# Kernel optimization log

Hardware: AMD Instinct MI355X
Metric: run time of the kernel (lower is better)

The kernel has to match this reference:

```python
import jax, jax.numpy as jnp
import numpy as np

H, DH = 8, 64          # num_heads, head_dim
DM = H * DH            # hidden_dim = 512
LAM = 1.0              # lambda_param
SCALE = 1.0 / np.sqrt(DH)


def setup_inputs() -> dict:
    key = jax.random.key(0)
    ks = jax.random.split(key, 12)
    B, N, R = 2, 2048, 16
    s = DM ** -0.5
    inp = {
        "x": jax.random.normal(ks[0], (B, N, DM), jnp.float32),
        "pde_residuals": jax.random.normal(ks[1], (B, N, R), jnp.float32),
        "mask": jnp.ones((B, 1, N, N), jnp.int32),
        "Wq": jax.random.normal(ks[2], (DM, DM), jnp.float32) * s,
        "bq": jax.random.normal(ks[3], (DM,), jnp.float32) * 0.01,
        "Wk": jax.random.normal(ks[4], (DM, DM), jnp.float32) * s,
        "bk": jax.random.normal(ks[5], (DM,), jnp.float32) * 0.01,
        "Wv": jax.random.normal(ks[6], (DM, DM), jnp.float32) * s,
        "bv": jax.random.normal(ks[7], (DM,), jnp.float32) * 0.01,
        "Wo": jax.random.normal(ks[8], (DM, DM), jnp.float32) * s,
        "bo": jax.random.normal(ks[9], (DM,), jnp.float32) * 0.01,
    }
    return inp


def reference(x, pde_residuals, mask, Wq, bq, Wk, bk, Wv, bv, Wo, bo):
    B, N, _ = x.shape
    # torch nn.Linear: y = x @ W.T + b
    q = (x @ Wq.T + bq).reshape(B, N, H, DH)
    k = (x @ Wk.T + bk).reshape(B, N, H, DH)
    v = (x @ Wv.T + bv).reshape(B, N, H, DH)
    # [B,H,N,N]
    scores = jnp.einsum('bqhd,bkhd->bhqk', q, k) * SCALE
    # residual bias: rb.unsqueeze(1) - rb.unsqueeze(2) -> bias[b,i,j] = rb[b,j] - rb[b,i]
    rb = jnp.linalg.norm(pde_residuals, axis=-1)            # [B,N]
    bias = rb[:, None, None, :] - rb[:, None, :, None]       # [B,1,N,N]
    scores = scores - LAM * bias
    scores = jnp.where(mask == 0, -jnp.inf, scores)
    attn = jax.nn.softmax(scores, axis=-1)                   # dropout is identity in eval
    out = jnp.einsum('bhqk,bkhd->bqhd', attn, v).reshape(B, N, DM)
    return out @ Wo.T + bo
```

## Files before the change

### kernel.cpp

```cpp
#include <hip/hip_runtime.h>
#include <hip/hip_bf16.h>
#include <math.h>

#define B_ 2
#define N_ 2048
#define H_ 8
#define DH_ 64
#define DM_ 512
#define R_ 16
#define LAM_ 1.0f
#define SCALE_ 0.125f

typedef unsigned short u16;
typedef unsigned int u32;
typedef u16 u16x4 __attribute__((ext_vector_type(4)));
typedef u16 u16x8 __attribute__((ext_vector_type(8)));
typedef __bf16 bf16x8 __attribute__((ext_vector_type(8)));
typedef float f32x4 __attribute__((ext_vector_type(4)));

static __device__ __forceinline__ u16 f2bf(float f) {
    union { float f; unsigned u; } v; v.f = f;
    unsigned r = v.u + 0x7FFF + ((v.u >> 16) & 1);
    return (u16)(r >> 16);
}

static __device__ __forceinline__ u32 pack_bf16(float lo, float hi) {
    float2 f2; f2.x = lo; f2.y = hi;
    __hip_bfloat162 h2 = __float22bfloat162_rn(f2);
    u32 r;
    __builtin_memcpy(&r, &h2, 4);
    return r;
}

static __device__ __forceinline__ void gl_lds16(const void* g, void* l) {
    __builtin_amdgcn_global_load_lds(
        (const __attribute__((address_space(1))) unsigned*)g,
        (__attribute__((address_space(3))) unsigned*)l, 16, 0, 0);
}

__global__ __launch_bounds__(256) void cast_all(
    const float* __restrict__ x, const float* __restrict__ wq,
    const float* __restrict__ wk, const float* __restrict__ wv,
    const float* __restrict__ wo, u16* __restrict__ xb, u16* __restrict__ wqb,
    u16* __restrict__ wkb, u16* __restrict__ wvb, u16* __restrict__ wob) {
    int y = blockIdx.y;
    const float* src; u16* dst; int n;
    switch (y) {
        case 0: src = x;  dst = xb;  n = 2097152; break;
        case 1: src = wq; dst = wqb; n = 262144;  break;
        case 2: src = wk; dst = wkb; n = 262144;  break;
        case 3: src = wv; dst = wvb; n = 262144;  break;
        default: src = wo; dst = wob; n = 262144; break;
    }
    int i = (blockIdx.x * 256 + threadIdx.x) * 8;
    if (i >= n) return;
    float4 a = *(const float4*)(src + i);
    float4 b = *(const float4*)(src + i + 4);
    u16x8 o;
    o[0] = f2bf(a.x); o[1] = f2bf(a.y); o[2] = f2bf(a.z); o[3] = f2bf(a.w);
    o[4] = f2bf(b.x); o[5] = f2bf(b.y); o[6] = f2bf(b.z); o[7] = f2bf(b.w);
    *(u16x8*)(dst + i) = o;
}

__global__ void rb_kernel(const float* __restrict__ pde, float* __restrict__ rbs) {
    int i = blockIdx.x * blockDim.x + threadIdx.x;
    if (i >= B_ * N_) return;
    const float4* p = (const float4*)(pde + (size_t)i * R_);
    float s = 0.f;
#pragma unroll
    for (int j = 0; j < 4; ++j) {
        float4 v = p[j];
        s += v.x * v.x + v.y * v.y + v.z * v.z + v.w * v.w;
    }
    rbs[i] = LAM_ * sqrtf(s);
}

__global__ __launch_bounds__(256) void mask_scan(const int* __restrict__ mask,
                                                 int* __restrict__ flags) {
    int kt = blockIdx.x, qt = blockIdx.y, b = blockIdx.z;
    __shared__ int red;
    if (threadIdx.x == 0) red = 0;
    __syncthreads();
    int any = 0;
    for (int c = threadIdx.x; c < 1024; c += 256) {
        int row = c >> 4, seg = c & 15;
        int4 m4 = *(const int4*)(mask + (size_t)b * N_ * N_ +
                                 (size_t)(qt * 64 + row) * N_ + kt * 64 + seg * 4);
        any |= (m4.x == 0) | (m4.y == 0) | (m4.z == 0) | (m4.w == 0);
    }
    if (__ballot(any)) {
        if ((threadIdx.x & 63) == 0) atomicOr(&red, 1);
    }
    __syncthreads();
    if (threadIdx.x == 0) flags[(b * 32 + qt) * 32 + kt] = red;
}

struct Acc2 { f32x4 v[4][2]; };

static __device__ __forceinline__ Acc2 gemm_core2(const u16* __restrict__ A,
                                                  const u16* __restrict__ W,
                                                  int m0, int nn0, char* LDSB) {
    int t = threadIdx.x, l = t & 63, w = t >> 6;
    int lg = l >> 4, li = l & 15;
    int wr = w >> 1, wc = w & 1;
    Acc2 acc;
#pragma unroll
    for (int m = 0; m < 4; ++m)
#pragma unroll
        for (int n = 0; n < 2; ++n) acc.v[m][n] = (f32x4){0.f, 0.f, 0.f, 0.f};

    int srl = l >> 3;
    int colb = ((l & 7) * 16) ^ (srl << 4);

    for (int k0 = 0; k0 < DM_; k0 += 64) {
        __syncthreads();
#pragma unroll
        for (int i = 0; i < 4; ++i) {
            int c = w * 4 + i;
            int row = c * 8 + srl;
            gl_lds16(A + (size_t)(m0 + row) * DM_ + k0 + (colb >> 1),
                     LDSB + c * 1024);
        }
#pragma unroll
        for (int i = 0; i < 2; ++i) {
            int c = w * 2 + i;
            int row = c * 8 + srl;
            gl_lds16(W + (size_t)(nn0 + row) * DM_ + k0 + (colb >> 1),
                     LDSB + 16384 + c * 1024);
        }
        __syncthreads();
#pragma unroll
        for (int kk = 0; kk < 2; ++kk) {
            bf16x8 af[4], bfr[2];
#pragma unroll
            for (int m = 0; m < 4; ++m) {
                int r = wr * 64 + m * 16 + li;
                af[m] = *(const bf16x8*)(LDSB + r * 128 +
                                         ((kk * 64 + lg * 16) ^ ((r & 7) << 4)));
            }
#pragma unroll
            for (int n = 0; n < 2; ++n) {
                int r = wc * 32 + n * 16 + li;
                bfr[n] = *(const bf16x8*)(LDSB + 16384 + r * 128 +
                                          ((kk * 64 + lg * 16) ^ ((r & 7) << 4)));
            }
#pragma unroll
            for (int m = 0; m < 4; ++m)
#pragma unroll
                for (int n = 0; n < 2; ++n)
                    acc.v[m][n] = __builtin_amdgcn_mfma_f32_16x16x32_bf16(
                        af[m], bfr[n], acc.v[m][n], 0, 0, 0);
        }
    }
    return acc;
}

__global__ __launch_bounds__(256) void gemm_qkv(
    const u16* __restrict__ xb, const u16* __restrict__ wqb,
    const u16* __restrict__ wkb, const u16* __restrict__ wvb,
    const float* __restrict__ bq, const float* __restrict__ bk,
    const float* __restrict__ bv, u16* __restrict__ q_bf,
    u16* __restrict__ k_bf, u16* __restrict__ vt) {
    __shared__ char LDSB[24576];
    int y = blockIdx.y;
    int which = y >> 3;
    int nn0 = (y & 7) * 64;
    const u16* W = which == 0 ? wqb : which == 1 ? wkb : wvb;
    const float* bias = which == 0 ? bq : which == 1 ? bk : bv;
    int m0 = blockIdx.x * 128;
    Acc2 acc = gemm_core2(xb, W, m0, nn0, LDSB);

    int t = threadIdx.x, l = t & 63, w = t >> 6;
    int lg = l >> 4, li = l & 15;
    int wr = w >> 1, wc = w & 1;
    float scale = which == 0 ? SCALE_ : 1.0f;
#pragma unroll
    for (int n = 0; n < 2; ++n) {
        int col = nn0 + wc * 32 + n * 16 + li;
        float bv_ = bias[col];
        if (which < 2) {
            u16* dst = which == 0 ? q_bf : k_bf;
#pragma unroll
            for (int m = 0; m < 4; ++m)
#pragma unroll
                for (int r = 0; r < 4; ++r) {
                    int row = m0 + wr * 64 + m * 16 + lg * 4 + r;
                    dst[(size_t)row * DM_ + col] =
                        f2bf((acc.v[m][n][r] + bv_) * scale);
                }
        } else {
            int h = col >> 6, d = col & 63;
#pragma unroll
            for (int m = 0; m < 4; ++m) {
                int row = m0 + wr * 64 + m * 16 + lg * 4;
                int b = row >> 11, nb = row & (N_ - 1);
                u16x4 o;
#pragma unroll
                for (int r = 0; r < 4; ++r) o[r] = f2bf(acc.v[m][n][r] + bv_);
                *(u16x4*)(vt + ((size_t)((b * 8 + h) * 64 + d)) * N_ + nb) = o;
            }
        }
    }
}

__global__ __launch_bounds__(256) void gemm_out(
    const u16* __restrict__ aob, const u16* __restrict__ wob,
    const float* __restrict__ bo, float* __restrict__ out) {
    __shared__ char LDSB[24576];
    int nn0 = blockIdx.y * 64;
    int m0 = blockIdx.x * 128;
    Acc2 acc = gemm_core2(aob, wob, m0, nn0, LDSB);

    int t = threadIdx.x, l = t & 63, w = t >> 6;
    int lg = l >> 4, li = l & 15;
    int wr = w >> 1, wc = w & 1;
#pragma unroll
    for (int n = 0; n < 2; ++n) {
        int col = nn0 + wc * 32 + n * 16 + li;
        float bv_ = bo[col];
#pragma unroll
        for (int m = 0; m < 4; ++m)
#pragma unroll
            for (int r = 0; r < 4; ++r) {
                int row = m0 + wr * 64 + m * 16 + lg * 4 + r;
                out[(size_t)row * DM_ + col] = acc.v[m][n][r] + bv_;
            }
    }
}

__global__ __launch_bounds__(512) void attn8(
    const u16* __restrict__ qb, const u16* __restrict__ kb,
    const u16* __restrict__ vtb, const float* __restrict__ rbs,
    const int* __restrict__ mask, const int* __restrict__ flags,
    u16* __restrict__ aob) {
    __shared__ char KVB[2][2][16384];
    __shared__ char PsB[8][2048];

    int t = threadIdx.x, l = t & 63, w = t >> 6;
    int g2 = w >> 2, wq = w & 3;
    int raw = blockIdx.x;
    int sid = (raw & 7) * 64 + (raw >> 3);
    int bh = sid >> 5, qg = sid & 31;
    int b = bh >> 3, h = bh & 7;
    int m0 = qg * 64 + wq * 16;
    int lg = l >> 4, li = l & 15;
    int k0base = g2 * 1024;

    int srl = l >> 3;
    int colb = ((l & 7) * 16) ^ (srl << 4);

    bf16x8 qa[2];
    {
        const u16* qrow = qb + (size_t)(b * N_ + m0 + li) * DM_ + h * DH_;
        qa[0] = __builtin_bit_cast(bf16x8, *(const u16x8*)(qrow + lg * 8));
        qa[1] = __builtin_bit_cast(bf16x8, *(const u16x8*)(qrow + 32 + lg * 8));
    }

    f32x4 o[4];
#pragma unroll
    for (int dt = 0; dt < 4; ++dt) o[dt] = (f32x4){0.f, 0.f, 0.f, 0.f};
    float mrun = -INFINITY, lrun = 0.f;

    auto STAGE = [&](int bufi, int k0s) {
        char* base = &KVB[g2][bufi][0];
#pragma unroll
        for (int c = 0; c < 2; ++c) {
            int chunk = wq * 2 + c;
            int row = chunk * 8 + srl;
            gl_lds16(kb + (size_t)(b * N_ + k0s + row) * DM_ + h * DH_ + (colb >> 1),
                     base + chunk * 1024);
            gl_lds16(vtb + ((size_t)(bh * DH_ + row)) * N_ + k0s + (colb >> 1),
                     base + 8192 + chunk * 1024);
        }
    };

    STAGE(0, k0base);
    __syncthreads();

    char* pwbase = &PsB[w][0] + li * 16 + ((lg & 1) << 3);
    int slot_lohi = (lg >> 1);

    int buf = 0;
    for (int tt = 0; tt < 16; ++tt) {
        int k0 = k0base + tt * 64;
        if (tt < 15) STAGE(buf ^ 1, k0 + 64);

        const char* Kb = &KVB[g2][buf][0];
        const char* Vb = &KVB[g2][buf][8192];
        int flag = flags[(b * 32 + qg) * 32 + (k0 >> 6)];

        f32x4 st[4];
        __builtin_amdgcn_s_setprio(1);
#pragma unroll
        for (int kt = 0; kt < 4; ++kt) {
            st[kt] = (f32x4){0.f, 0.f, 0.f, 0.f};
#pragma unroll
            for (int s = 0; s < 2; ++s) {
                int key = kt * 16 + li;
                bf16x8 kf = *(const bf16x8*)(Kb + key * 128 +
                                             ((s * 64 + lg * 16) ^ ((key & 7) << 4)));
                st[kt] = __builtin_amdgcn_mfma_f32_16x16x32_bf16(kf, qa[s], st[kt],
                                                                 0, 0, 0);
            }
        }
        __builtin_amdgcn_s_setprio(0);

#pragma unroll
        for (int kt = 0; kt < 4; ++kt) {
            float4 rb4 = *(const float4*)(rbs + b * N_ + k0 + kt * 16 + lg * 4);
            st[kt][0] -= rb4.x; st[kt][1] -= rb4.y;
            st[kt][2] -= rb4.z; st[kt][3] -= rb4.w;
        }
        if (flag) {
#pragma unroll
            for (int kt = 0; kt < 4; ++kt)
#pragma unroll
                for (int r = 0; r < 4; ++r) {
                    int rowg = m0 + li;
                    int keyg = k0 + kt * 16 + lg * 4 + r;
                    if (mask[(size_t)b * N_ * N_ + (size_t)rowg * N_ + keyg] == 0)
                        st[kt][r] = -INFINITY;
                }
        }

        float m0_ = fmaxf(fmaxf(st[0][0], st[0][1]), fmaxf(st[0][2], st[0][3]));
        float m1_ = fmaxf(fmaxf(st[1][0], st[1][1]), fmaxf(st[1][2], st[1][3]));
        float m2_ = fmaxf(fmaxf(st[2][0], st[2][1]), fmaxf(st[2][2], st[2][3]));
        float m3_ = fmaxf(fmaxf(st[3][0], st[3][1]), fmaxf(st[3][2], st[3][3]));
        float pmax = fmaxf(fmaxf(m0_, m1_), fmaxf(m2_, m3_));
        pmax = fmaxf(pmax, __shfl_xor(pmax, 16));
        pmax = fmaxf(pmax, __shfl_xor(pmax, 32));

        if (!__all(pmax - mrun <= 8.0f)) {
            float mnew = fmaxf(fmaxf(mrun, pmax), -3.0e38f);
            float corr = __expf(mrun - mnew);
            mrun = mnew;
            lrun *= corr;
#pragma unroll
            for (int dt = 0; dt < 4; ++dt)
#pragma unroll
                for (int r = 0; r < 4; ++r) o[dt][r] *= corr;
        }

        float ps[8];
#pragma unroll
        for (int kt = 0; kt < 4; ++kt) {
            float p0 = __expf(st[kt][0] - mrun);
            float p1 = __expf(st[kt][1] - mrun);
            float p2 = __expf(st[kt][2] - mrun);
            float p3 = __expf(st[kt][3] - mrun);
            ps[kt * 2 + 0] = p0 + p1;
            ps[kt * 2 + 1] = p2 + p3;
            uint2 pkw;
            pkw.x = pack_bf16(p0, p1);
            pkw.y = pack_bf16(p2, p3);
            int slot = (kt >> 1) * 4 + (kt & 1) * 2 + slot_lohi;
            *(uint2*)(pwbase + (slot << 8)) = pkw;
        }
        float psum = ((ps[0] + ps[1]) + (ps[2] + ps[3])) +
                     ((ps[4] + ps[5]) + (ps[6] + ps[7]));
        psum += __shfl_xor(psum, 16);
        psum += __shfl_xor(psum, 32);
        lrun += psum;

        bf16x8 pf[2];
#pragma unroll
        for (int s = 0; s < 2; ++s)
            pf[s] = *(const bf16x8*)(&PsB[w][0] + ((s * 4 + lg) << 8) + li * 16);
        __builtin_amdgcn_s_setprio(1);
#pragma unroll
        for (int dt = 0; dt < 4; ++dt)
#pragma unroll
            for (int s = 0; s < 2; ++s) {
                int d = dt * 16 + li;
                bf16x8 vf = *(const bf16x8*)(Vb + d * 128 +
                                             ((s * 64 + lg * 16) ^ ((d & 7) << 4)));
                o[dt] = __builtin_amdgcn_mfma_f32_16x16x32_bf16(vf, pf[s], o[dt],
                                                                0, 0, 0);
            }
        __builtin_amdgcn_s_setprio(0);

        __syncthreads();
        buf ^= 1;
    }

    float* cmb = (float*)&KVB[0][0][0];
    float* mlc = (float*)&PsB[0][0];
    if (g2 == 1) {
        float* dst = cmb + wq * 1024;
#pragma unroll
        for (int dt = 0; dt < 4; ++dt)
            *(f32x4*)(dst + li * 64 + dt * 16 + lg * 4) = o[dt];
        if (lg == 0) {
            float2 ml; ml.x = mrun; ml.y = lrun;
            *(float2*)(mlc + (wq * 16 + li) * 2) = ml;
        }
    }
    __syncthreads();
    if (g2 == 0) {
        float2 ml1 = *(const float2*)(mlc + (wq * 16 + li) * 2);
        float m = fmaxf(mrun, ml1.x);
        float w0 = __expf(mrun - m), w1 = __expf(ml1.x - m);
        float denom = 1.f / (lrun * w0 + ml1.y * w1);
        w0 *= denom; w1 *= denom;
        const float* src = cmb + wq * 1024;
        u16* orow = aob + (size_t)(b * N_ + m0 + li) * DM_ + h * DH_;
#pragma unroll
        for (int dt = 0; dt < 4; ++dt) {
            f32x4 p1 = *(const f32x4*)(src + li * 64 + dt * 16 + lg * 4);
            u16x4 ov;
#pragma unroll
            for (int r = 0; r < 4; ++r)
                ov[r] = f2bf(o[dt][r] * w0 + p1[r] * w1);
            *(u16x4*)(orow + dt * 16 + lg * 4) = ov;
        }
    }
}

extern "C" void kernel_launch(void* const* d_in, const int* in_sizes, int n_in,
                              void* d_out, int out_size, void* d_ws, size_t ws_size,
                              hipStream_t stream) {
    const float* x   = (const float*)d_in[0];
    const float* pde = (const float*)d_in[1];
    const int*   msk = (const int*)d_in[2];
    const float* Wq  = (const float*)d_in[3];
    const float* bq  = (const float*)d_in[4];
    const float* Wk  = (const float*)d_in[5];
    const float* bk  = (const float*)d_in[6];
    const float* Wv  = (const float*)d_in[7];
    const float* bv  = (const float*)d_in[8];
    const float* Wo  = (const float*)d_in[9];
    const float* bo  = (const float*)d_in[10];
    float* out = (float*)d_out;

    const size_t MAT = (size_t)B_ * N_ * DM_;
    const size_t WSZ = (size_t)DM_ * DM_;
    u16* xb   = (u16*)d_ws;
    u16* q_bf = xb + MAT;
    u16* k_bf = q_bf + MAT;
    u16* vt   = k_bf + MAT;
    u16* aob  = vt + MAT;
    u16* wqb  = aob + MAT;
    u16* wkb  = wqb + WSZ;
    u16* wvb  = wkb + WSZ;
    u16* wob  = wvb + WSZ;
    float* rbs = (float*)(wob + WSZ);
    int* flags = (int*)(rbs + B_ * N_);

    cast_all<<<dim3(1024, 5), 256, 0, stream>>>(x, Wq, Wk, Wv, Wo,
                                                xb, wqb, wkb, wvb, wob);
    rb_kernel<<<(B_ * N_ + 255) / 256, 256, 0, stream>>>(pde, rbs);
    mask_scan<<<dim3(32, 32, 2), 256, 0, stream>>>(msk, flags);

    gemm_qkv<<<dim3(32, 24), 256, 0, stream>>>(xb, wqb, wkb, wvb,
                                               bq, bk, bv, q_bf, k_bf, vt);

    attn8<<<512, 512, 0, stream>>>(q_bf, k_bf, vt, rbs, msk, flags, aob);

    gemm_out<<<dim3(32, 8), 256, 0, stream>>>(aob, wob, bo, out);
}
```

Baseline: 76.93 us.

## Fuse prep kernels into one launch, shrink output GEMM tile, pad combine LDS

The cast, residual-norm and mask-scan kernels are merged into a single prep launch dispatched by blockIdx.y, which removes two kernel launches and their gaps. The output projection GEMM now uses a 64x64 tile with a new gemm_core, doubling the grid from 256 to 512 blocks so more CUs are busy. The attention combine buffer gets a row stride of 68 floats instead of 64 to reduce LDS bank conflicts. Smaller GEMM tiles cut per-block data reuse, and the fused prep kernel launches blocks that exit immediately in the mostly empty y rows.

```diff
diff --git a/kernel.cpp b/kernel.cpp
--- a/kernel.cpp
+++ b/kernel.cpp
@@ -38,61 +38,117 @@
         (__attribute__((address_space(3))) unsigned*)l, 16, 0, 0);
 }
 
-__global__ __launch_bounds__(256) void cast_all(
+__global__ __launch_bounds__(256) void prep(
     const float* __restrict__ x, const float* __restrict__ wq,
     const float* __restrict__ wk, const float* __restrict__ wv,
-    const float* __restrict__ wo, u16* __restrict__ xb, u16* __restrict__ wqb,
-    u16* __restrict__ wkb, u16* __restrict__ wvb, u16* __restrict__ wob) {
-    int y = blockIdx.y;
-    const float* src; u16* dst; int n;
-    switch (y) {
-        case 0: src = x;  dst = xb;  n = 2097152; break;
-        case 1: src = wq; dst = wqb; n = 262144;  break;
-        case 2: src = wk; dst = wkb; n = 262144;  break;
-        case 3: src = wv; dst = wvb; n = 262144;  break;
-        default: src = wo; dst = wob; n = 262144; break;
-    }
-    int i = (blockIdx.x * 256 + threadIdx.x) * 8;
-    if (i >= n) return;
-    float4 a = *(const float4*)(src + i);
-    float4 b = *(const float4*)(src + i + 4);
-    u16x8 o;
-    o[0] = f2bf(a.x); o[1] = f2bf(a.y); o[2] = f2bf(a.z); o[3] = f2bf(a.w);
-    o[4] = f2bf(b.x); o[5] = f2bf(b.y); o[6] = f2bf(b.z); o[7] = f2bf(b.w);
-    *(u16x8*)(dst + i) = o;
-}
-
-__global__ void rb_kernel(const float* __restrict__ pde, float* __restrict__ rbs) {
-    int i = blockIdx.x * blockDim.x + threadIdx.x;
-    if (i >= B_ * N_) return;
-    const float4* p = (const float4*)(pde + (size_t)i * R_);
-    float s = 0.f;
-#pragma unroll
-    for (int j = 0; j < 4; ++j) {
-        float4 v = p[j];
-        s += v.x * v.x + v.y * v.y + v.z * v.z + v.w * v.w;
-    }
-    rbs[i] = LAM_ * sqrtf(s);
-}
-
-__global__ __launch_bounds__(256) void mask_scan(const int* __restrict__ mask,
-                                                 int* __restrict__ flags) {
-    int kt = blockIdx.x, qt = blockIdx.y, b = blockIdx.z;
-    __shared__ int red;
-    if (threadIdx.x == 0) red = 0;
-    __syncthreads();
-    int any = 0;
-    for (int c = threadIdx.x; c < 1024; c += 256) {
-        int row = c >> 4, seg = c & 15;
-        int4 m4 = *(const int4*)(mask + (size_t)b * N_ * N_ +
-                                 (size_t)(qt * 64 + row) * N_ + kt * 64 + seg * 4);
-        any |= (m4.x == 0) | (m4.y == 0) | (m4.z == 0) | (m4.w == 0);
-    }
-    if (__ballot(any)) {
-        if ((threadIdx.x & 63) == 0) atomicOr(&red, 1);
-    }
-    __syncthreads();
-    if (threadIdx.x == 0) flags[(b * 32 + qt) * 32 + kt] = red;
+    const float* __restrict__ wo, const float* __restrict__ pde,
+    const int* __restrict__ mask, u16* __restrict__ xb, u16* __restrict__ wqb,
+    u16* __restrict__ wkb, u16* __restrict__ wvb, u16* __restrict__ wob,
+    float* __restrict__ rbs, int* __restrict__ flags) {
+    int y = blockIdx.y, bx = blockIdx.x, t = threadIdx.x;
+
+    if (y <= 4) {
+        const float* src; u16* dst; int n;
+        switch (y) {
+            case 0: src = x;  dst = xb;  n = 2097152; break;
+            case 1: src = wq; dst = wqb; n = 262144;  break;
+            case 2: src = wk; dst = wkb; n = 262144;  break;
+            case 3: src = wv; dst = wvb; n = 262144;  break;
+            default: src = wo; dst = wob; n = 262144; break;
+        }
+        int i = (bx * 256 + t) * 8;
+        if (i >= n) return;
+        float4 a = *(const float4*)(src + i);
+        float4 b = *(const float4*)(src + i + 4);
+        u16x8 o;
+        o[0] = f2bf(a.x); o[1] = f2bf(a.y); o[2] = f2bf(a.z); o[3] = f2bf(a.w);
+        o[4] = f2bf(b.x); o[5] = f2bf(b.y); o[6] = f2bf(b.z); o[7] = f2bf(b.w);
+        *(u16x8*)(dst + i) = o;
+    } else if (y == 5) {
+        int i = bx * 256 + t;
+        if (i >= B_ * N_) return;
+        const float4* p = (const float4*)(pde + (size_t)i * R_);
+        float s = 0.f;
+#pragma unroll
+        for (int j = 0; j < 4; ++j) {
+            float4 v = p[j];
+            s += v.x * v.x + v.y * v.y + v.z * v.z + v.w * v.w;
+        }
+        rbs[i] = LAM_ * sqrtf(s);
+    } else {
+        int b = y - 6;
+        int qt = bx >> 5, kt = bx & 31;
+        __shared__ int red;
+        if (t == 0) red = 0;
+        __syncthreads();
+        int any = 0;
+        for (int c = t; c < 1024; c += 256) {
+            int row = c >> 4, seg = c & 15;
+            int4 m4 = *(const int4*)(mask + (size_t)b * N_ * N_ +
+                                     (size_t)(qt * 64 + row) * N_ + kt * 64 + seg * 4);
+            any |= (m4.x == 0) | (m4.y == 0) | (m4.z == 0) | (m4.w == 0);
+        }
+        if (__ballot(any)) {
+            if ((t & 63) == 0) atomicOr(&red, 1);
+        }
+        __syncthreads();
+        if (t == 0) flags[(b * 32 + qt) * 32 + kt] = red;
+    }
+}
+
+struct Acc { f32x4 v[2][2]; };
+
+static __device__ __forceinline__ Acc gemm_core(const u16* __restrict__ A,
+                                                const u16* __restrict__ W,
+                                                int m0, int nn0, char* LDSB) {
+    int t = threadIdx.x, l = t & 63, w = t >> 6;
+    int lg = l >> 4, li = l & 15;
+    int wr = w >> 1, wc = w & 1;
+    Acc acc;
+#pragma unroll
+    for (int m = 0; m < 2; ++m)
+#pragma unroll
+        for (int n = 0; n < 2; ++n) acc.v[m][n] = (f32x4){0.f, 0.f, 0.f, 0.f};
+
+    int srl = l >> 3;
+    int colb = ((l & 7) * 16) ^ (srl << 4);
+
+    for (int k0 = 0; k0 < DM_; k0 += 64) {
+        __syncthreads();
+#pragma unroll
+        for (int i = 0; i < 2; ++i) {
+            int c = w * 2 + i;
+            int row = c * 8 + srl;
+            gl_lds16(A + (size_t)(m0 + row) * DM_ + k0 + (colb >> 1),
+                     LDSB + c * 1024);
+            gl_lds16(W + (size_t)(nn0 + row) * DM_ + k0 + (colb >> 1),
+                     LDSB + 8192 + c * 1024);
+        }
+        __syncthreads();
+#pragma unroll
+        for (int kk = 0; kk < 2; ++kk) {
+            bf16x8 af[2], bfr[2];
+#pragma unroll
+            for (int m = 0; m < 2; ++m) {
+                int r = wr * 32 + m * 16 + li;
+                af[m] = *(const bf16x8*)(LDSB + r * 128 +
+                                         ((kk * 64 + lg * 16) ^ ((r & 7) << 4)));
+            }
+#pragma unroll
+            for (int n = 0; n < 2; ++n) {
+                int r = wc * 32 + n * 16 + li;
+                bfr[n] = *(const bf16x8*)(LDSB + 8192 + r * 128 +
+                                          ((kk * 64 + lg * 16) ^ ((r & 7) << 4)));
+            }
+#pragma unroll
+            for (int m = 0; m < 2; ++m)
+#pragma unroll
+                for (int n = 0; n < 2; ++n)
+                    acc.v[m][n] = __builtin_amdgcn_mfma_f32_16x16x32_bf16(
+                        af[m], bfr[n], acc.v[m][n], 0, 0, 0);
+        }
+    }
+    return acc;
 }
 
 struct Acc2 { f32x4 v[4][2]; };
@@ -208,8 +264,8 @@
     const float* __restrict__ bo, float* __restrict__ out) {
     __shared__ char LDSB[24576];
     int nn0 = blockIdx.y * 64;
-    int m0 = blockIdx.x * 128;
-    Acc2 acc = gemm_core2(aob, wob, m0, nn0, LDSB);
+    int m0 = blockIdx.x * 64;
+    Acc acc = gemm_core(aob, wob, m0, nn0, LDSB);
 
     int t = threadIdx.x, l = t & 63, w = t >> 6;
     int lg = l >> 4, li = l & 15;
@@ -219,10 +275,10 @@
         int col = nn0 + wc * 32 + n * 16 + li;
         float bv_ = bo[col];
 #pragma unroll
-        for (int m = 0; m < 4; ++m)
+        for (int m = 0; m < 2; ++m)
 #pragma unroll
             for (int r = 0; r < 4; ++r) {
-                int row = m0 + wr * 64 + m * 16 + lg * 4 + r;
+                int row = m0 + wr * 32 + m * 16 + lg * 4 + r;
                 out[(size_t)row * DM_ + col] = acc.v[m][n][r] + bv_;
             }
     }
@@ -387,10 +443,10 @@
     float* cmb = (float*)&KVB[0][0][0];
     float* mlc = (float*)&PsB[0][0];
     if (g2 == 1) {
-        float* dst = cmb + wq * 1024;
+        float* dst = cmb + wq * 1088;
 #pragma unroll
         for (int dt = 0; dt < 4; ++dt)
-            *(f32x4*)(dst + li * 64 + dt * 16 + lg * 4) = o[dt];
+            *(f32x4*)(dst + li * 68 + dt * 16 + lg * 4) = o[dt];
         if (lg == 0) {
             float2 ml; ml.x = mrun; ml.y = lrun;
             *(float2*)(mlc + (wq * 16 + li) * 2) = ml;
@@ -403,11 +459,11 @@
         float w0 = __expf(mrun - m), w1 = __expf(ml1.x - m);
         float denom = 1.f / (lrun * w0 + ml1.y * w1);
         w0 *= denom; w1 *= denom;
-        const float* src = cmb + wq * 1024;
+        const float* src = cmb + wq * 1088;
         u16* orow = aob + (size_t)(b * N_ + m0 + li) * DM_ + h * DH_;
 #pragma unroll
         for (int dt = 0; dt < 4; ++dt) {
-            f32x4 p1 = *(const f32x4*)(src + li * 64 + dt * 16 + lg * 4);
+            f32x4 p1 = *(const f32x4*)(src + li * 68 + dt * 16 + lg * 4);
             u16x4 ov;
 #pragma unroll
             for (int r = 0; r < 4; ++r)
@@ -447,15 +503,13 @@
     float* rbs = (float*)(wob + WSZ);
     int* flags = (int*)(rbs + B_ * N_);
 
-    cast_all<<<dim3(1024, 5), 256, 0, stream>>>(x, Wq, Wk, Wv, Wo,
-                                                xb, wqb, wkb, wvb, wob);
-    rb_kernel<<<(B_ * N_ + 255) / 256, 256, 0, stream>>>(pde, rbs);
-    mask_scan<<<dim3(32, 32, 2), 256, 0, stream>>>(msk, flags);
+    prep<<<dim3(1024, 8), 256, 0, stream>>>(x, Wq, Wk, Wv, Wo, pde, msk,
+                                            xb, wqb, wkb, wvb, wob, rbs, flags);
 
     gemm_qkv<<<dim3(32, 24), 256, 0, stream>>>(xb, wqb, wkb, wvb,
                                                bq, bk, bv, q_bf, k_bf, vt);
 
     attn8<<<512, 512, 0, stream>>>(q_bf, k_bf, vt, rbs, msk, flags, aob);
 
-    gemm_out<<<dim3(32, 8), 256, 0, stream>>>(aob, wob, bo, out);
-}
+    gemm_out<<<dim3(64, 8), 256, 0, stream>>>(aob, wob, bo, out);
+}
```

Result: faster. 70.13 us (-8.8%).
